# Kernel optimization log

Hardware: AMD Instinct MI355X
Metric: run time of the kernel (lower is better)

Reference implementation:

```python
import jax, jax.numpy as jnp
import numpy as np

B, S, IN, H, OUT, L = 32, 512, 300, 180, 60, 4
NBLOCK, NF = 3, 3  # mel_smooth_layers, mel_smooth_filter_size
GRP = OUT // NF    # 20 groups per mel conv


def setup_inputs() -> dict:
    key = jax.random.key(0)
    ks = jax.random.split(key, 12)
    def u(k, shape, scale):
        return jax.random.uniform(k, shape, jnp.float32, -scale, scale)
    s = float(1.0 / np.sqrt(H))
    return {
        "x": jax.random.normal(ks[0], (B, S, IN), jnp.float32),
        "Wih0": u(ks[1], (4 * H, IN), s),
        "Wih_rest": u(ks[2], (L - 1, 4 * H, H), s),
        "Whh": u(ks[3], (L, 4 * H, H), s),
        "bih": u(ks[4], (L, 4 * H), s),
        "bhh": u(ks[5], (L, 4 * H), s),
        "linW": u(ks[6], (OUT, H), s),
        "linb": u(ks[7], (OUT,), s),
        "mel_w": u(ks[8], (NBLOCK, NF, GRP, NF, 5), 0.2),  # per block, per filter: Conv1d(60,20,5,groups=20)
        "mel_b": u(ks[9], (NBLOCK, NF, GRP), 0.2),
        "resW": u(ks[10], (OUT, 2, 5), 0.2),               # Conv1d(120,60,5,groups=60)
        "resb": u(ks[11], (OUT,), 0.2),
    }


def _lstm(x, Wih0, Wih_rest, Whh, bih, bhh):
    # torch nn.LSTM, batch_first, gate order (i, f, g, o)
    h_in = x  # [B, S, D]
    for l in range(L):
        Wih = Wih0 if l == 0 else Wih_rest[l - 1]
        Whh_l = Whh[l]
        b = bih[l] + bhh[l]
        xt = h_in.transpose(1, 0, 2) @ Wih.T + b  # [S, B, 4H], input projection hoisted out of scan
        def step(carry, xg):
            h, c = carry
            g = xg + h @ Whh_l.T
            i, f, gg, o = jnp.split(g, 4, axis=-1)
            c = jax.nn.sigmoid(f) * c + jax.nn.sigmoid(i) * jnp.tanh(gg)
            h = jax.nn.sigmoid(o) * jnp.tanh(c)
            return (h, c), h
        init = (jnp.zeros((x.shape[0], H), x.dtype), jnp.zeros((x.shape[0], H), x.dtype))
        _, hs = jax.lax.scan(step, init, xt)  # [S, B, H]
        h_in = hs.transpose(1, 0, 2)
    return h_in  # [B, S, H]


def _conv1d_grouped(x, w, b, groups):
    # x: [B, C, S], w: [O, C//groups, K]
    y = jax.lax.conv_general_dilated(
        x, w, window_strides=(1,), padding=[(2, 2)],
        dimension_numbers=("NCH", "OIH", "NCH"), feature_group_count=groups)
    return y + b[None, :, None]


def _mel_block(x, w, b):
    # x: [B, 60, S]; w: [NF, 20, NF, 5]; b: [NF, 20]
    Bb, C, Ss = x.shape
    z = jnp.zeros((Bb, 1, Ss), x.dtype)
    # shifted channel stacks: [down-shift-1, identity, up-shift-1] (filter_size_channel == 3)
    xs = [jnp.concatenate([z, x[:, :-1]], axis=1), x, jnp.concatenate([x[:, 1:], z], axis=1)]
    outs = [_conv1d_grouped(xs[j], w[j], b[j], GRP) for j in range(NF)]  # each [B, 20, S]
    # interleave: output channel 3*i + j = outs[j][:, i, :]
    return jnp.stack(outs, axis=2).reshape(Bb, C, Ss)


def _forward(x, Wih0, Wih_rest, Whh, bih, bhh, linW, linb, mel_w, mel_b, resW, resb):
    h = _lstm(x, Wih0, Wih_rest, Whh, bih, bhh)      # [B, S, H]
    out = h @ linW.T + linb                          # [B, S, 60]
    out = out.transpose(0, 2, 1)                     # [B, 60, S]
    lstm_out = out
    for l in range(NBLOCK):
        out = _mel_block(out, mel_w[l], mel_b[l]) + out  # block + shortcut (Identity activation)
    # interleave (lstm, smoothed) per mel channel -> [B, 120, S]
    pair = jnp.stack([lstm_out, out], axis=2).reshape(out.shape[0], 2 * OUT, out.shape[2])
    out = _conv1d_grouped(pair, resW, resb, OUT)     # [B, 60, S]
    return out.transpose(0, 2, 1)                    # [B, S, 60] (Identity output activation)


def reference(x, Wih0, Wih_rest, Whh, bih, bhh, linW, linb, mel_w, mel_b, resW, resb):
    return _forward(x, Wih0, Wih_rest, Whh, bih, bhh, linW, linb, mel_w, mel_b, resW, resb)
```

## Files before the change

### kernel.cpp

```cpp
#include <hip/hip_runtime.h>
#include <hip/hip_bf16.h>

#define B_ 32
#define S_ 512
#define IN_ 300
#define H_ 180
#define G4_ 720
#define OUT_ 60
#define R_ 16384
#define TC_ 32
#define NC_ 16
#define NPK_ 92

#define PWHH_O  0u
#define PW0_O   264960u
#define PWR_O   372960u
#define BIASF_O 567360u
#define LINWF_O 570240u
#define LINBF_O 581040u
#define WFT_    581100u

#define XG_O   0u
#define HR_O   5898240u
#define H3_O   7004160u
#define WFU_O  8478720u
#define STH_O  9059820u
#define STC_O  9082860u
#define FLAG_O 9105900u
#define XGSLOT 737280
#define HRSLOT 184320

#if defined(__has_builtin)
#if __has_builtin(__builtin_amdgcn_fdot2)
#define HAVE_FDOT2 1
#endif
#endif

typedef _Float16 f16x2 __attribute__((ext_vector_type(2)));

struct Plan {
  int nl; int ll[4]; int lc[4];
  int ng; int gl[4]; int gc[4];
};

__device__ __forceinline__ float sigf(float x)   { return 1.f / (1.f + __expf(-x)); }
__device__ __forceinline__ float tanhf2(float x) { return 2.f / (1.f + __expf(-2.f * x)) - 1.f; }
__device__ __forceinline__ float toF(__hip_bfloat16 x) { return __bfloat162float(x); }
__device__ __forceinline__ float ldr(const void* p, long i, int fl) {
  return fl ? ((const float*)p)[i] : toF(((const __hip_bfloat16*)p)[i]);
}
__device__ __forceinline__ unsigned f16b(_Float16 h) {
  union { _Float16 f; unsigned short s; } x; x.f = h; return x.s;
}
__device__ __forceinline__ float h2f(unsigned s) {
  union { unsigned short s; _Float16 f; } x; x.s = (unsigned short)(s & 0xFFFFu);
  return (float)x.f;
}
__device__ __forceinline__ f16x2 u2h(unsigned u) {
  union { unsigned u; f16x2 v; } x; x.u = u; return x.v;
}
__device__ __forceinline__ float fd2(unsigned hu, unsigned wu, float acc) {
#ifdef HAVE_FDOT2
  return __builtin_amdgcn_fdot2(u2h(hu), u2h(wu), acc, false);
#else
  return acc + h2f(hu) * h2f(wu) + h2f(hu >> 16) * h2f(wu >> 16);
#endif
}
__device__ __forceinline__ unsigned packpair_f32(float lo, float hi) {
  return f16b((_Float16)lo) | (f16b((_Float16)hi) << 16);
}
__device__ __forceinline__ unsigned packpair_bf16(unsigned u) {
  union { unsigned v; float f; } a, b;
  a.v = u << 16; b.v = u & 0xFFFF0000u;
  return packpair_f32(a.f, b.f);
}

#define REP23(M) M(0) M(1) M(2) M(3) M(4) M(5) M(6) M(7) M(8) M(9) M(10) \
  M(11) M(12) M(13) M(14) M(15) M(16) M(17) M(18) M(19) M(20) M(21) M(22)
#define LW(n) \
  unsigned w##n##a = wp0[(4*n+0)*G4_], w##n##b = wp0[(4*n+1)*G4_], \
           w##n##c = wp0[(4*n+2)*G4_], w##n##d = wp0[(4*n+3)*G4_];
#define PW(n) \
  asm volatile("" : "+v"(w##n##a), "+v"(w##n##b), "+v"(w##n##c), "+v"(w##n##d));
#define ST(n) { \
  const uint4 hh = *(const uint4*)&hpk[4*n]; \
  a0 = fd2(hh.x, w##n##a, a0); a1 = fd2(hh.y, w##n##b, a1); \
  a2 = fd2(hh.z, w##n##c, a2); a3 = fd2(hh.w, w##n##d, a3); }

__global__ __launch_bounds__(256) void detect_kernel(
    const unsigned short* __restrict__ xw, int* __restrict__ flag) {
  __shared__ int cnt;
  if (threadIdx.x == 0) cnt = 0;
  __syncthreads();
  int lc = 0;
  for (int i = threadIdx.x; i < 2048; i += 256) {
    const int e = (xw[i] >> 7) & 0xFF;
    if (e >= 0xC0 || (e > 0 && e < 0x40)) lc++;
  }
  atomicAdd(&cnt, lc);
  __syncthreads();
  if (threadIdx.x == 0) *flag = (cnt > 100) ? 1 : 0;
}

__global__ __launch_bounds__(256) void prep_kernel(
    const void* __restrict__ wih0, const void* __restrict__ wihr,
    const void* __restrict__ whh,  const void* __restrict__ bih,
    const void* __restrict__ bhh,  const void* __restrict__ linw,
    const void* __restrict__ linb, float* __restrict__ wf,
    const int* __restrict__ flag) {
  const unsigned i = blockIdx.x * 256u + threadIdx.x;
  if (i >= WFT_) return;
  const int fl = *flag;
  if (i < PW0_O) {
    const unsigned l = i / 66240u, r = i % 66240u;
    const unsigned jp = r / 720u, o = r % 720u;
    unsigned u = 0u;
    if (jp < 90u) {
      const long b = (long)l * 129600 + (long)o * H_;
      u = packpair_f32(ldr(whh, b + 2 * jp, fl), ldr(whh, b + 2 * jp + 1, fl));
    }
    ((unsigned*)wf)[i] = u;
    return;
  }
  if (i < PWR_O) {
    const unsigned j = i - PW0_O, o = j / 150u, kp = j % 150u;
    const long b = (long)o * IN_;
    ((unsigned*)wf)[i] =
        packpair_f32(ldr(wih0, b + 2 * kp, fl), ldr(wih0, b + 2 * kp + 1, fl));
    return;
  }
  if (i < BIASF_O) {
    const unsigned j = i - PWR_O, l = j / 64800u, r = j % 64800u;
    const unsigned o = r / 90u, kp = r % 90u;
    const long b = (long)l * 129600 + (long)o * H_;
    ((unsigned*)wf)[i] =
        packpair_f32(ldr(wihr, b + 2 * kp, fl), ldr(wihr, b + 2 * kp + 1, fl));
    return;
  }
  float v;
  if (i < LINWF_O)      { const unsigned j = i - BIASF_O; v = ldr(bih, j, fl) + ldr(bhh, j, fl); }
  else if (i < LINBF_O) v = ldr(linw, i - LINWF_O, fl);
  else                  v = ldr(linb, i - LINBF_O, fl);
  wf[i] = v;
}

__global__ __launch_bounds__(768, 3) void fused_kernel(
    const void* __restrict__ x, const int* __restrict__ flag,
    const unsigned* __restrict__ wfu,
    float* __restrict__ xg, float* __restrict__ hr,
    __hip_bfloat16* __restrict__ h3,
    float* __restrict__ sth, float* __restrict__ stc, Plan p) {
  __shared__ __align__(16) unsigned hpk[NPK_];
  __shared__ float gbuf[G4_];
  __shared__ __align__(16) unsigned Asu[3][10][68];
  __shared__ __align__(16) unsigned Bsu[3][10][68];

  const int bid = blockIdx.x;
  if (bid < p.nl * 32) {
    const int j = bid >> 5, b = bid & 31;
    const int l = p.ll[j], c = p.lc[j];
    const int o = threadIdx.x;
    const bool act = o < G4_;
    const int oc = act ? o : 0;
    const unsigned* wp0 = wfu + PWHH_O + (unsigned)l * (NPK_ * G4_) + oc;
    REP23(LW)
    REP23(PW)
    const float* xgs = xg + (long)(l * 2 + (c & 1)) * XGSLOT;
    float* hrs = hr + (long)((l < 3 ? l : 0) * 2 + (c & 1)) * HRSLOT;
    float cst = 0.f;
    if (o == 180 || o == 181) hpk[o - 90] = 0u;
    if (o < H_) {
      float h = 0.f;
      if (c != 0) { h = sth[(l * 32 + b) * H_ + o]; cst = stc[(l * 32 + b) * H_ + o]; }
      const unsigned v = f16b((_Float16)h);
      const unsigned nx = __shfl_down(v, 1);
      if ((o & 1) == 0) hpk[o >> 1] = v | (nx << 16);
    }
    const float* xgp = xgs + (long)b * TC_ * G4_ + oc;
    float xcur = xgp[0];
    __syncthreads();
    for (int tl = 0; tl < TC_; ++tl) {
      {
        float a0 = xcur, a1 = 0.f, a2 = 0.f, a3 = 0.f;
        REP23(ST)
        const float acc = (a0 + a1) + (a2 + a3);
        const bool isg = (o >= 2 * H_) && (o < 3 * H_);
        if (act) gbuf[o] = isg ? tanhf2(acc) : sigf(acc);
        const int tn = (tl + 1 < TC_) ? tl + 1 : tl;
        xcur = xgp[(long)tn * G4_];
      }
      asm volatile("s_waitcnt lgkmcnt(0)\n\ts_barrier" ::: "memory");
      if (o < H_) {
        cst = gbuf[H_ + o] * cst + gbuf[o] * gbuf[2 * H_ + o];
        const float h = gbuf[3 * H_ + o] * tanhf2(cst);
        if (l < 3) hrs[(b * TC_ + tl) * H_ + o] = h;
        else h3[((long)b * S_ + c * TC_ + tl) * H_ + o] = __float2bfloat16(h);
        const unsigned v = f16b((_Float16)h);
        const unsigned nx = __shfl_down(v, 1);
        if ((o & 1) == 0) hpk[o >> 1] = v | (nx << 16);
        if (tl == TC_ - 1) {
          sth[(l * 32 + b) * H_ + o] = h; stc[(l * 32 + b) * H_ + o] = cst;
        }
      }
      asm volatile("s_waitcnt lgkmcnt(0)\n\ts_barrier" ::: "memory");
    }
    return;
  }

  const int gb = bid - p.nl * 32;
  const int g = threadIdx.x >> 8, t = threadIdx.x & 255;
  const int ti = gb * 3 + g;
  const int jj = ti / 192, idx = ti % 192;
  const int rt = idx & 15, ct = idx >> 4;
  const int l = p.gl[jj], c = p.gc[jj];
  const int fl = *flag;
  const int KP = (l == 0) ? 150 : 90;
  const unsigned* Wp = (l == 0) ? (wfu + PW0_O)
                                : (wfu + PWR_O + (unsigned)(l - 1) * 64800u);
  const float* bias = (const float*)wfu + BIASF_O + (unsigned)l * G4_;
  const float* hA = (l == 0) ? nullptr
                  : hr + (long)((l - 1) * 2 + (c & 1)) * HRSLOT;
  float* dst = xg + (long)(l * 2 + (c & 1)) * XGSLOT;
  const int rho0 = rt * 64, o0 = ct * 64;
  const int tx = t & 15, ty = t >> 4;
  float acc[4][4] = {};
  for (int kp0 = 0; kp0 < KP; kp0 += 10) {
    for (int e = t; e < 640; e += 256) {
      const int rl = e / 10, pp = e % 10;
      const int rho = rho0 + rl;
      unsigned av;
      if (l == 0) {
        const int bb = rho >> 5, tl = rho & 31;
        const long gr = (long)bb * S_ + c * TC_ + tl;
        if (fl == 0) av = packpair_bf16(((const unsigned*)x)[gr * 150 + kp0 + pp]);
        else { const float2 f = ((const float2*)x)[gr * 150 + kp0 + pp];
               av = packpair_f32(f.x, f.y); }
      } else {
        const float2 f = ((const float2*)hA)[(long)rho * 90 + kp0 + pp];
        av = packpair_f32(f.x, f.y);
      }
      Asu[g][pp][rl] = av;
      const int o = o0 + rl;
      Bsu[g][pp][rl] = (o < G4_) ? Wp[(long)o * KP + kp0 + pp] : 0u;
    }
    __syncthreads();
#pragma unroll
    for (int pp = 0; pp < 10; ++pp) {
      const uint4 a4 = *(const uint4*)&Asu[g][pp][ty * 4];
      const uint4 b4 = *(const uint4*)&Bsu[g][pp][tx * 4];
      const unsigned av[4] = {a4.x, a4.y, a4.z, a4.w};
      const unsigned bv[4] = {b4.x, b4.y, b4.z, b4.w};
#pragma unroll
      for (int i = 0; i < 4; ++i)
#pragma unroll
        for (int j2 = 0; j2 < 4; ++j2) acc[i][j2] = fd2(av[i], bv[j2], acc[i][j2]);
    }
    __syncthreads();
  }
#pragma unroll
  for (int i = 0; i < 4; ++i) {
    const int rho = rho0 + ty * 4 + i;
#pragma unroll
    for (int j2 = 0; j2 < 4; ++j2) {
      const int o = o0 + tx * 4 + j2;
      if (o < G4_) dst[(long)rho * G4_ + o] = acc[i][j2] + bias[o];
    }
  }
}

__global__ __launch_bounds__(256) void linear_kernel(
    const __hip_bfloat16* __restrict__ h, const float* __restrict__ linw,
    const float* __restrict__ linb, float* __restrict__ out) {
  __shared__ __align__(16) float Ast[20][68];
  __shared__ __align__(16) float Bst[20][68];
  const int bt = blockIdx.x;
  const int b = bt >> 3, st0 = (bt & 7) * 64;
  const int t = threadIdx.x, tx = t & 15, ty = t >> 4;
  float acc[4][4] = {};
  for (int k0 = 0; k0 < H_; k0 += 20) {
    for (int e = t; e < 1280; e += 256) {
      const int rl = e / 20, kk = e % 20;
      Ast[kk][rl] = toF(h[(long)(b * S_ + st0 + rl) * H_ + k0 + kk]);
      Bst[kk][rl] = (rl < OUT_) ? linw[rl * H_ + k0 + kk] : 0.f;
    }
    __syncthreads();
#pragma unroll
    for (int kk = 0; kk < 20; ++kk) {
      const float4 a4 = *(const float4*)&Ast[kk][ty * 4];
      const float4 b4 = *(const float4*)&Bst[kk][tx * 4];
      const float av[4] = {a4.x, a4.y, a4.z, a4.w};
      const float bv[4] = {b4.x, b4.y, b4.z, b4.w};
#pragma unroll
      for (int i = 0; i < 4; ++i)
#pragma unroll
        for (int j2 = 0; j2 < 4; ++j2) acc[i][j2] += av[i] * bv[j2];
    }
    __syncthreads();
  }
#pragma unroll
  for (int i = 0; i < 4; ++i) {
    const int s = st0 + ty * 4 + i;
#pragma unroll
    for (int j2 = 0; j2 < 4; ++j2) {
      const int c = tx * 4 + j2;
      if (c < OUT_) out[((long)b * OUT_ + c) * S_ + s] = acc[i][j2] + linb[c];
    }
  }
}

__global__ __launch_bounds__(256) void mel_kernel(
    const float* __restrict__ in, float* __restrict__ out,
    const void* __restrict__ mw, const void* __restrict__ mb,
    int l, const int* __restrict__ flag) {
  const int fl = *flag;
  const int idx = blockIdx.x;
  const int s = (idx & 1) * 256 + threadIdx.x;
  const int c = (idx >> 1) % OUT_;
  const int b = idx / (2 * OUT_);
  const int j = c % 3, i = c / 3;
  float acc = ldr(mb, (l * 3 + j) * 20 + i, fl);
  const long wbase = (long)((l * 3 + j) * 20 + i) * 15;
#pragma unroll
  for (int q = 0; q < 3; ++q) {
    const int ch = 3 * i + q + j - 1;
    if (ch < 0 || ch >= OUT_) continue;
    const float* xr = in + ((long)b * OUT_ + ch) * S_;
#pragma unroll
    for (int k = 0; k < 5; ++k) {
      const int sp = s + k - 2;
      if (sp < 0 || sp >= S_) continue;
      acc += ldr(mw, wbase + q * 5 + k, fl) * xr[sp];
    }
  }
  out[((long)b * OUT_ + c) * S_ + s] = acc + in[((long)b * OUT_ + c) * S_ + s];
}

__global__ __launch_bounds__(256) void res_kernel(
    const float* __restrict__ lin, const float* __restrict__ mel,
    const void* __restrict__ rw, const void* __restrict__ rb,
    void* __restrict__ outp, const int* __restrict__ flag) {
  const int fl = *flag;
  const int q = threadIdx.x >> 6, lane = threadIdx.x & 63;
  const int bs = blockIdx.x * 4 + q;
  const int b = bs / S_, s = bs % S_;
  if (lane >= OUT_) return;
  const int c = lane;
  float acc = ldr(rb, c, fl);
  const float* x0 = lin + ((long)b * OUT_ + c) * S_;
  const float* x1 = mel + ((long)b * OUT_ + c) * S_;
#pragma unroll
  for (int k = 0; k < 5; ++k) {
    const int sp = s + k - 2;
    if (sp < 0 || sp >= S_) continue;
    acc += ldr(rw, c * 10 + k, fl) * x0[sp] + ldr(rw, c * 10 + 5 + k, fl) * x1[sp];
  }
  const long oi = (long)bs * OUT_ + c;
  if (fl == 0) ((__hip_bfloat16*)outp)[oi] = __float2bfloat16(acc);
  else ((float*)outp)[oi] = acc;
}

extern "C" void kernel_launch(void* const* d_in, const int* in_sizes, int n_in,
                              void* d_out, int out_size, void* d_ws, size_t ws_size,
                              hipStream_t stream) {
  const void* x    = d_in[0];
  const void* wih0 = d_in[1];
  const void* wihr = d_in[2];
  const void* whh  = d_in[3];
  const void* bih  = d_in[4];
  const void* bhh  = d_in[5];
  const void* linw = d_in[6];
  const void* linb = d_in[7];
  const void* melw = d_in[8];
  const void* melb = d_in[9];
  const void* resw = d_in[10];
  const void* resb = d_in[11];

  float* ws = (float*)d_ws;
  float* xg = ws + XG_O;
  float* hrp = ws + HR_O;
  __hip_bfloat16* h3 = (__hip_bfloat16*)(ws + H3_O);
  float* wf = ws + WFU_O;
  const unsigned* wfu = (const unsigned*)wf;
  float* sth = ws + STH_O;
  float* stc = ws + STC_O;
  int* flag = (int*)(ws + FLAG_O);
  float* lin = ws + XG_O;
  float* m1 = lin + 983040;
  float* m2 = m1 + 983040;

  detect_kernel<<<1, 256, 0, stream>>>((const unsigned short*)x, flag);
  prep_kernel<<<(WFT_ + 255) / 256, 256, 0, stream>>>(
      wih0, wihr, whh, bih, bhh, linw, linb, wf, flag);

  {
    Plan p = {};
    p.nl = 0; p.ng = 1; p.gl[0] = 0; p.gc[0] = 0;
    fused_kernel<<<64, 768, 0, stream>>>(x, flag, wfu, xg, hrp, h3, sth, stc, p);
  }
  for (int n = 0; n <= 21; ++n) {
    Plan p = {};
    for (int l = 0; l < 4; ++l) {
      const int c = n - 2 * l;
      if (c >= 0 && c < NC_) { p.ll[p.nl] = l; p.lc[p.nl] = c; p.nl++; }
    }
    for (int l = 0; l < 4; ++l) {
      const int c = n + 1 - 2 * l;
      if (c >= 0 && c < NC_) { p.gl[p.ng] = l; p.gc[p.ng] = c; p.ng++; }
    }
    const int grid = p.nl * 32 + p.ng * 64;
    fused_kernel<<<grid, 768, 0, stream>>>(x, flag, wfu, xg, hrp, h3, sth, stc, p);
  }

  linear_kernel<<<256, 256, 0, stream>>>(h3, wf + LINWF_O, wf + LINBF_O, lin);
  mel_kernel<<<B_ * OUT_ * 2, 256, 0, stream>>>(lin, m1, melw, melb, 0, flag);
  mel_kernel<<<B_ * OUT_ * 2, 256, 0, stream>>>(m1, m2, melw, melb, 1, flag);
  mel_kernel<<<B_ * OUT_ * 2, 256, 0, stream>>>(m2, m1, melw, melb, 2, flag);
  res_kernel<<<R_ / 4, 256, 0, stream>>>(lin, m1, resw, resb, d_out, flag);
}
```

Measured before the change: 1.512 ms.

## Process two batch rows per LSTM block with gate-interleaved layout and DPP gate exchange

Each recurrent block now handles two batch elements, reusing the register-resident Whh weights for both dot products and halving the number of LSTM blocks. Gate rows are reordered so the four gates of each hidden unit sit in adjacent lanes, which lets the cell update exchange gate values with DPP quad broadcasts instead of going through a shared gate buffer. The hidden state is double-buffered in LDS, so each timestep needs one barrier instead of two. The input projection writes in the new interleaved layout with a padded 768 stride. The trade-off is double the per-thread dot-product work on each serial step and fewer active blocks.

```diff
diff --git a/kernel.cpp b/kernel.cpp
--- a/kernel.cpp
+++ b/kernel.cpp
@@ -21,18 +21,21 @@
 #define WFT_    581100u
 
 #define XG_O   0u
-#define HR_O   5898240u
-#define H3_O   7004160u
-#define WFU_O  8478720u
-#define STH_O  9059820u
-#define STC_O  9082860u
-#define FLAG_O 9105900u
-#define XGSLOT 737280
+#define HR_O   6291456u
+#define H3_O   7397376u
+#define WFU_O  8871936u
+#define STH_O  9453036u
+#define STC_O  9476076u
+#define FLAG_O 9499116u
+#define XGSLOT 786432
 #define HRSLOT 184320
 
 #if defined(__has_builtin)
 #if __has_builtin(__builtin_amdgcn_fdot2)
 #define HAVE_FDOT2 1
+#endif
+#if __has_builtin(__builtin_amdgcn_mov_dpp)
+#define HAVE_DPP 1
 #endif
 #endif
 
@@ -74,6 +77,14 @@
   a.v = u << 16; b.v = u & 0xFFFF0000u;
   return packpair_f32(a.f, b.f);
 }
+
+#ifdef HAVE_DPP
+#define QBC(dst, src, J) { \
+  const int qv_ = __builtin_amdgcn_mov_dpp(__float_as_int(src), (J) * 85, 0xF, 0xF, false); \
+  dst = __int_as_float(qv_); }
+#else
+#define QBC(dst, src, J) dst = __shfl(src, (((threadIdx.x & 63) & ~3) + (J)), 64);
+#endif
 
 #define REP23(M) M(0) M(1) M(2) M(3) M(4) M(5) M(6) M(7) M(8) M(9) M(10) \
   M(11) M(12) M(13) M(14) M(15) M(16) M(17) M(18) M(19) M(20) M(21) M(22)
@@ -82,10 +93,13 @@
            w##n##c = wp0[(4*n+2)*G4_], w##n##d = wp0[(4*n+3)*G4_];
 #define PW(n) \
   asm volatile("" : "+v"(w##n##a), "+v"(w##n##b), "+v"(w##n##c), "+v"(w##n##d));
-#define ST(n) { \
-  const uint4 hh = *(const uint4*)&hpk[4*n]; \
-  a0 = fd2(hh.x, w##n##a, a0); a1 = fd2(hh.y, w##n##b, a1); \
-  a2 = fd2(hh.z, w##n##c, a2); a3 = fd2(hh.w, w##n##d, a3); }
+#define ST2(n) { \
+  const uint4 hA_ = *(const uint4*)&hbA[4*n]; \
+  const uint4 hB_ = *(const uint4*)&hbB[4*n]; \
+  aA0 = fd2(hA_.x, w##n##a, aA0); aA1 = fd2(hA_.y, w##n##b, aA1); \
+  aA2 = fd2(hA_.z, w##n##c, aA2); aA3 = fd2(hA_.w, w##n##d, aA3); \
+  aB0 = fd2(hB_.x, w##n##a, aB0); aB1 = fd2(hB_.y, w##n##b, aB1); \
+  aB2 = fd2(hB_.z, w##n##c, aB2); aB3 = fd2(hB_.w, w##n##d, aB3); }
 
 __global__ __launch_bounds__(256) void detect_kernel(
     const unsigned short* __restrict__ xw, int* __restrict__ flag) {
@@ -114,9 +128,10 @@
   if (i < PW0_O) {
     const unsigned l = i / 66240u, r = i % 66240u;
     const unsigned jp = r / 720u, o = r % 720u;
+    const unsigned ro = (o & 3u) * 180u + (o >> 2);
     unsigned u = 0u;
     if (jp < 90u) {
-      const long b = (long)l * 129600 + (long)o * H_;
+      const long b = (long)l * 129600 + (long)ro * H_;
       u = packpair_f32(ldr(whh, b + 2 * jp, fl), ldr(whh, b + 2 * jp + 1, fl));
     }
     ((unsigned*)wf)[i] = u;
@@ -150,56 +165,86 @@
     float* __restrict__ xg, float* __restrict__ hr,
     __hip_bfloat16* __restrict__ h3,
     float* __restrict__ sth, float* __restrict__ stc, Plan p) {
-  __shared__ __align__(16) unsigned hpk[NPK_];
-  __shared__ float gbuf[G4_];
+  __shared__ __align__(16) unsigned hpk[2][2][NPK_];
   __shared__ __align__(16) unsigned Asu[3][10][68];
   __shared__ __align__(16) unsigned Bsu[3][10][68];
 
   const int bid = blockIdx.x;
-  if (bid < p.nl * 32) {
-    const int j = bid >> 5, b = bid & 31;
+  if (bid < p.nl * 16) {
+    const int j = bid >> 4, pb = bid & 15;
     const int l = p.ll[j], c = p.lc[j];
+    const int b0 = pb * 2, b1 = b0 + 1;
     const int o = threadIdx.x;
-    const bool act = o < G4_;
-    const int oc = act ? o : 0;
+    const int oc = (o < G4_) ? o : (G4_ - 1);
+    const int g = o & 3, u = o >> 2;
+    const bool act = (o < G4_);
     const unsigned* wp0 = wfu + PWHH_O + (unsigned)l * (NPK_ * G4_) + oc;
     REP23(LW)
     REP23(PW)
     const float* xgs = xg + (long)(l * 2 + (c & 1)) * XGSLOT;
     float* hrs = hr + (long)((l < 3 ? l : 0) * 2 + (c & 1)) * HRSLOT;
-    float cst = 0.f;
-    if (o == 180 || o == 181) hpk[o - 90] = 0u;
-    if (o < H_) {
-      float h = 0.f;
-      if (c != 0) { h = sth[(l * 32 + b) * H_ + o]; cst = stc[(l * 32 + b) * H_ + o]; }
-      const unsigned v = f16b((_Float16)h);
-      const unsigned nx = __shfl_down(v, 1);
-      if ((o & 1) == 0) hpk[o >> 1] = v | (nx << 16);
-    }
-    const float* xgp = xgs + (long)b * TC_ * G4_ + oc;
-    float xcur = xgp[0];
+    float cstA = 0.f, cstB = 0.f, hA0 = 0.f, hB0 = 0.f;
+    if (c != 0 && act) {
+      cstA = stc[(l * 32 + b0) * H_ + u]; hA0 = sth[(l * 32 + b0) * H_ + u];
+      cstB = stc[(l * 32 + b1) * H_ + u]; hB0 = sth[(l * 32 + b1) * H_ + u];
+    }
+    if (o < 4 * NPK_ && (o % NPK_) >= (NPK_ - 2)) ((unsigned*)hpk)[o] = 0u;
+    {
+      const unsigned vA = f16b((_Float16)hA0);
+      const unsigned nA = __shfl_down(vA, 4);
+      const unsigned vB = f16b((_Float16)hB0);
+      const unsigned nB = __shfl_down(vB, 4);
+      if (act && (o & 7) == 0) {
+        hpk[0][0][u >> 1] = vA | (nA << 16);
+        hpk[1][0][u >> 1] = vB | (nB << 16);
+      }
+    }
+    const float* xpA = xgs + (long)b0 * TC_ * 768 + o;
+    const float* xpB = xgs + (long)b1 * TC_ * 768 + o;
+    float xcA = xpA[0], xcB = xpB[0];
+    const float sg = (g == 2) ? 2.f : 1.f;
     __syncthreads();
     for (int tl = 0; tl < TC_; ++tl) {
-      {
-        float a0 = xcur, a1 = 0.f, a2 = 0.f, a3 = 0.f;
-        REP23(ST)
-        const float acc = (a0 + a1) + (a2 + a3);
-        const bool isg = (o >= 2 * H_) && (o < 3 * H_);
-        if (act) gbuf[o] = isg ? tanhf2(acc) : sigf(acc);
-        const int tn = (tl + 1 < TC_) ? tl + 1 : tl;
-        xcur = xgp[(long)tn * G4_];
+      const unsigned* hbA = hpk[0][tl & 1];
+      const unsigned* hbB = hpk[1][tl & 1];
+      float aA0 = xcA, aA1 = 0.f, aA2 = 0.f, aA3 = 0.f;
+      float aB0 = xcB, aB1 = 0.f, aB2 = 0.f, aB3 = 0.f;
+      REP23(ST2)
+      const float accA = (aA0 + aA1) + (aA2 + aA3);
+      const float accB = (aB0 + aB1) + (aB2 + aB3);
+      const int tn = (tl + 1 < TC_) ? tl + 1 : tl;
+      xcA = xpA[(long)tn * 768]; xcB = xpB[(long)tn * 768];
+      const float vA_ = 1.f / (1.f + __expf(-sg * accA));
+      const float gvA = fmaf(sg, vA_ - 1.f, 1.f);
+      const float vB_ = 1.f / (1.f + __expf(-sg * accB));
+      const float gvB = fmaf(sg, vB_ - 1.f, 1.f);
+      float qiA, qfA, qgA, qoA, qiB, qfB, qgB, qoB;
+      QBC(qiA, gvA, 0) QBC(qfA, gvA, 1) QBC(qgA, gvA, 2) QBC(qoA, gvA, 3)
+      QBC(qiB, gvB, 0) QBC(qfB, gvB, 1) QBC(qgB, gvB, 2) QBC(qoB, gvB, 3)
+      cstA = qfA * cstA + qiA * qgA;
+      cstB = qfB * cstB + qiB * qgB;
+      const float hA = qoA * tanhf2(cstA);
+      const float hB = qoB * tanhf2(cstB);
+      const unsigned vA = f16b((_Float16)hA);
+      const unsigned nA = __shfl_down(vA, 4);
+      const unsigned vB = f16b((_Float16)hB);
+      const unsigned nB = __shfl_down(vB, 4);
+      const int wb = (tl & 1) ^ 1;
+      if (act && (o & 7) == 0) {
+        hpk[0][wb][u >> 1] = vA | (nA << 16);
+        hpk[1][wb][u >> 1] = vB | (nB << 16);
       }
-      asm volatile("s_waitcnt lgkmcnt(0)\n\ts_barrier" ::: "memory");
-      if (o < H_) {
-        cst = gbuf[H_ + o] * cst + gbuf[o] * gbuf[2 * H_ + o];
-        const float h = gbuf[3 * H_ + o] * tanhf2(cst);
-        if (l < 3) hrs[(b * TC_ + tl) * H_ + o] = h;
-        else h3[((long)b * S_ + c * TC_ + tl) * H_ + o] = __float2bfloat16(h);
-        const unsigned v = f16b((_Float16)h);
-        const unsigned nx = __shfl_down(v, 1);
-        if ((o & 1) == 0) hpk[o >> 1] = v | (nx << 16);
+      if (act && g == 0) {
+        if (l < 3) {
+          hrs[(b0 * TC_ + tl) * H_ + u] = hA;
+          hrs[(b1 * TC_ + tl) * H_ + u] = hB;
+        } else {
+          h3[((long)b0 * S_ + c * TC_ + tl) * H_ + u] = __float2bfloat16(hA);
+          h3[((long)b1 * S_ + c * TC_ + tl) * H_ + u] = __float2bfloat16(hB);
+        }
         if (tl == TC_ - 1) {
-          sth[(l * 32 + b) * H_ + o] = h; stc[(l * 32 + b) * H_ + o] = cst;
+          sth[(l * 32 + b0) * H_ + u] = hA; stc[(l * 32 + b0) * H_ + u] = cstA;
+          sth[(l * 32 + b1) * H_ + u] = hB; stc[(l * 32 + b1) * H_ + u] = cstB;
         }
       }
       asm volatile("s_waitcnt lgkmcnt(0)\n\ts_barrier" ::: "memory");
@@ -207,7 +252,7 @@
     return;
   }
 
-  const int gb = bid - p.nl * 32;
+  const int gb = bid - p.nl * 16;
   const int g = threadIdx.x >> 8, t = threadIdx.x & 255;
   const int ti = gb * 3 + g;
   const int jj = ti / 192, idx = ti % 192;
@@ -263,7 +308,10 @@
 #pragma unroll
     for (int j2 = 0; j2 < 4; ++j2) {
       const int o = o0 + tx * 4 + j2;
-      if (o < G4_) dst[(long)rho * G4_ + o] = acc[i][j2] + bias[o];
+      if (o < G4_) {
+        const int gi = o / 180, un = o - gi * 180;
+        dst[(long)rho * 768 + un * 4 + gi] = acc[i][j2] + bias[o];
+      }
     }
   }
 }
@@ -407,7 +455,7 @@
       const int c = n + 1 - 2 * l;
       if (c >= 0 && c < NC_) { p.gl[p.ng] = l; p.gc[p.ng] = c; p.ng++; }
     }
-    const int grid = p.nl * 32 + p.ng * 64;
+    const int grid = p.nl * 16 + p.ng * 64;
     fused_kernel<<<grid, 768, 0, stream>>>(x, flag, wfu, xg, hrp, h3, sth, stc, p);
   }
 
```

Result: slower. 1.766 ms (+16.8%).
